# Kernel optimization log

Measured on AMD Instinct MI355X. Metric: run time of the kernel, lower is better.

Reference implementation:

```python
import jax, jax.numpy as jnp
import numpy as np

N_NODES = 100000
IN_DIM = 128
HID = 128
N_REL = 2
N_EDGES = 500000


def setup_inputs() -> dict:
    key = jax.random.key(0)
    ks = jax.random.split(key, 12)
    x = jax.random.normal(ks[0], (N_NODES, IN_DIM), dtype=jnp.float32)
    edge_index = jax.random.randint(ks[1], (2, N_EDGES), 0, N_NODES, dtype=jnp.int64)
    edge_type = jax.random.randint(ks[2], (N_EDGES,), 0, N_REL, dtype=jnp.int64)
    def w(k, shape, fan_in):
        return jax.random.normal(k, shape, dtype=jnp.float32) / np.sqrt(fan_in)
    return {
        "x": x,
        "edge_index": edge_index,
        "edge_type": edge_type,
        "W_rel1": w(ks[3], (N_REL, IN_DIM, HID), IN_DIM),
        "W_root1": w(ks[4], (IN_DIM, HID), IN_DIM),
        "b1": jnp.zeros((HID,), jnp.float32),
        "W_rel2": w(ks[5], (N_REL, HID, HID), HID),
        "W_root2": w(ks[6], (HID, HID), HID),
        "b2": jnp.zeros((HID,), jnp.float32),
        "Wc": w(ks[7], (HID, 2), HID),
        "bc": jnp.zeros((2,), jnp.float32),
    }


def rgcn_conv(x, src, dst, edge_type, W_rel, W_root, b, n_nodes):
    """PyG RGCNConv: out_i = x_i @ W_root + b + sum_r mean_{j in N_r(i)} x_j @ W_r."""
    out = x @ W_root + b
    for r in range(W_rel.shape[0]):  # small fixed relation count
        mask = (edge_type == r).astype(x.dtype)  # [E]
        xr = x @ W_rel[r]                         # [N, dout] transform-then-gather
        msg = xr[src] * mask[:, None]             # [E, dout]
        agg = jax.ops.segment_sum(msg, dst, num_segments=n_nodes)   # [N, dout]
        cnt = jax.ops.segment_sum(mask, dst, num_segments=n_nodes)  # [N]
        out = out + agg / jnp.maximum(cnt, 1.0)[:, None]            # mean aggr
    return out


def reference(x, edge_index, edge_type, W_rel1, W_root1, b1, W_rel2, W_root2, b2, Wc, bc):
    n = x.shape[0]
    src, dst = edge_index[0], edge_index[1]
    h = rgcn_conv(x, src, dst, edge_type, W_rel1, W_root1, b1, n)
    h = jax.nn.relu(h)
    # dropout is identity at inference (training=False)
    h = rgcn_conv(h, src, dst, edge_type, W_rel2, W_root2, b2, n)
    h = jax.nn.relu(h)
    logits = h @ Wc + bc
    return logits
```

## Files before the change

### kernel.cpp

```cpp
#include <hip/hip_runtime.h>
#include <hip/hip_fp16.h>

#define N_NODES 100000
#define PAD_N   100096
#define IN_DIM 128
#define HID 128
#define N_REL 2
#define N_EDGES 500000
#define M_SEG (N_REL * N_NODES)
#define SCAN_BLK 1024
#define SCAN_NB ((M_SEG + SCAN_BLK - 1) / SCAN_BLK)

#define CVT_BLOCKS 12500
#define PACK_BLOCKS 48
#define HIST_BLOCKS 1954

typedef __attribute__((ext_vector_type(8))) _Float16 half8;
typedef __attribute__((ext_vector_type(4))) float float4v;

__device__ __forceinline__ unsigned short f2h(float f) {
    return __half_as_ushort(__float2half(f));
}

__global__ __launch_bounds__(256) void prep_kernel(
    const float* __restrict__ X, unsigned short* __restrict__ Xb,
    const float* __restrict__ Wroot1, const float* __restrict__ Wrel1,
    const float* __restrict__ Wroot2, const float* __restrict__ Wrel2,
    unsigned short* __restrict__ Wp,
    const int* __restrict__ ei, const int* __restrict__ et,
    unsigned* __restrict__ cnt)
{
    int bid = blockIdx.x;
    if (bid < CVT_BLOCKS) {
        int i = bid * 256 + threadIdx.x;
        if (i >= N_NODES * IN_DIM / 4) return;
        float4 v = ((const float4*)X)[i];
        ushort4 o;
        o.x = f2h(v.x); o.y = f2h(v.y); o.z = f2h(v.z); o.w = f2h(v.w);
        ((ushort4*)Xb)[i] = o;
    } else if (bid < CVT_BLOCKS + PACK_BLOCKS) {
        int tid = (bid - CVT_BLOCKS) * 256 + threadIdx.x;
        int layer = tid / 6144;
        int rem   = tid % 6144;
        int ks    = rem / 512;
        int rem2  = rem % 512;
        int nt    = rem2 / 64;
        int lane  = rem2 % 64;
        int seg = ks >> 2;
        int kl  = (ks & 3) * 32 + (lane >> 4) * 8;
        int chan = nt * 16 + (lane & 15);
        const float* Wroot = layer ? Wroot2 : Wroot1;
        const float* Wrel  = layer ? Wrel2  : Wrel1;
        const float* W = (seg == 0) ? Wroot : (Wrel + (size_t)(seg - 1) * 128 * 128);
        unsigned short* dst = Wp + (size_t)tid * 8;
        #pragma unroll
        for (int j = 0; j < 8; ++j)
            dst[j] = f2h(W[(size_t)(kl + j) * 128 + chan]);
    } else {
        int e = (bid - CVT_BLOCKS - PACK_BLOCKS) * 256 + threadIdx.x;
        if (e >= N_EDGES) return;
        int dst = ei[N_EDGES + e];
        int r = et[e];
        atomicAdd(cnt + (size_t)r * N_NODES + dst, 1u);
    }
}

__global__ __launch_bounds__(256) void scan1_kernel(
    const unsigned* __restrict__ cnt,
    unsigned* __restrict__ rs, unsigned* __restrict__ bsums)
{
    __shared__ unsigned sdata[256];
    int t = threadIdx.x;
    int base = blockIdx.x * SCAN_BLK + t * 4;
    unsigned v[4]; unsigned s = 0;
    #pragma unroll
    for (int j = 0; j < 4; ++j) {
        v[j] = (base + j < M_SEG) ? cnt[base + j] : 0u;
        s += v[j];
    }
    sdata[t] = s;
    __syncthreads();
    #pragma unroll
    for (int off = 1; off < 256; off <<= 1) {
        unsigned x = (t >= off) ? sdata[t - off] : 0u;
        __syncthreads();
        if (t >= off) sdata[t] += x;
        __syncthreads();
    }
    unsigned excl = (t > 0) ? sdata[t - 1] : 0u;
    if (t == 255) bsums[blockIdx.x] = sdata[255];
    unsigned run = excl;
    #pragma unroll
    for (int j = 0; j < 4; ++j) {
        if (base + j < M_SEG) rs[base + j] = run;
        run += v[j];
    }
}

__global__ __launch_bounds__(256) void scan2_kernel(unsigned* __restrict__ bsums)
{
    __shared__ unsigned sdata[256];
    int t = threadIdx.x;
    sdata[t] = (t < SCAN_NB) ? bsums[t] : 0u;
    __syncthreads();
    #pragma unroll
    for (int off = 1; off < 256; off <<= 1) {
        unsigned x = (t >= off) ? sdata[t - off] : 0u;
        __syncthreads();
        if (t >= off) sdata[t] += x;
        __syncthreads();
    }
    if (t < SCAN_NB) bsums[t] = (t > 0) ? sdata[t - 1] : 0u;
}

__global__ __launch_bounds__(256) void scan3_kernel(
    unsigned* __restrict__ rs, const unsigned* __restrict__ bsums,
    unsigned* __restrict__ cursor)
{
    int i = blockIdx.x * blockDim.x + threadIdx.x;
    if (i < M_SEG) {
        unsigned v = rs[i] + bsums[i >> 10];
        rs[i] = v;
        cursor[i] = v;
    }
    if (i == 0) rs[M_SEG] = N_EDGES;
}

__global__ __launch_bounds__(256) void fill_kernel(
    const int* __restrict__ ei, const int* __restrict__ et,
    unsigned* __restrict__ cursor, unsigned* __restrict__ csr)
{
    int e = blockIdx.x * blockDim.x + threadIdx.x;
    if (e >= N_EDGES) return;
    int src = ei[e];
    int dst = ei[N_EDGES + e];
    int r = et[e];
    unsigned pos = atomicAdd(cursor + (size_t)r * N_NODES + dst, 1u);
    csr[pos] = (unsigned)src;
}

template <bool FINAL>
__global__ __launch_bounds__(256) void gemm_kernel(
    const unsigned short* __restrict__ Xin,
    const unsigned* __restrict__ rs,
    const unsigned* __restrict__ csr,
    const unsigned short* __restrict__ Wp,
    const float* __restrict__ bias,
    unsigned short* __restrict__ Hout,
    const float* __restrict__ Wc,
    const float* __restrict__ bc,
    float* __restrict__ Out)
{
    const int t    = threadIdx.x;
    const int w    = t >> 6;
    const int lane = t & 63;
    const int l15  = lane & 15;
    const int quad = lane >> 4;
    const int rowbase = blockIdx.x * 64 + w * 16;
    const int koff = quad * 8;

    const uint4* __restrict__ X4 = (const uint4*)Xin;

    const int node = rowbase + l15;
    unsigned p_[2], e_[2]; float inv_[2];
    #pragma unroll
    for (int r = 0; r < 2; ++r) {
        unsigned st = 0, en = 0;
        if (node < N_NODES) {
            unsigned sg = (unsigned)r * N_NODES + (unsigned)node;
            st = rs[sg];
            en = rs[sg + 1];
        }
        p_[r] = st; e_[r] = en;
        unsigned d = en - st;
        inv_[r] = 1.0f / (float)(d ? d : 1u);
    }

    __half2 a2[2][4][4];
    #pragma unroll
    for (int r = 0; r < 2; ++r)
        #pragma unroll
        for (int ksl = 0; ksl < 4; ++ksl)
            #pragma unroll
            for (int j = 0; j < 4; ++j)
                a2[r][ksl][j] = __float2half2_rn(0.f);

    const __half2 one2  = __float2half2_rn(1.f);
    const __half2 zero2 = __float2half2_rn(0.f);

    unsigned id[2][2];
    #pragma unroll
    for (int r = 0; r < 2; ++r)
        #pragma unroll
        for (int s = 0; s < 2; ++s) {
            unsigned q = p_[r] + (unsigned)s;
            id[r][s] = csr[q < e_[r] ? q : 0u];
        }

    while (__any((p_[0] < e_[0]) | (p_[1] < e_[1]))) {
        bool act[2][2];
        #pragma unroll
        for (int r = 0; r < 2; ++r)
            #pragma unroll
            for (int s = 0; s < 2; ++s)
                act[r][s] = (p_[r] + (unsigned)s) < e_[r];

        uint4 v[2][2][4];
        #pragma unroll
        for (int r = 0; r < 2; ++r)
            #pragma unroll
            for (int s = 0; s < 2; ++s) {
                const uint4* row = X4 +
                    ((size_t)(act[r][s] ? id[r][s] : 0u) << 4) + quad;
                v[r][s][0] = row[0];
                v[r][s][1] = row[4];
                v[r][s][2] = row[8];
                v[r][s][3] = row[12];
            }

        unsigned pn[2];
        #pragma unroll
        for (int r = 0; r < 2; ++r) {
            unsigned q = p_[r] + 2u;
            pn[r] = q > e_[r] ? e_[r] : q;
        }
        unsigned idn[2][2];
        #pragma unroll
        for (int r = 0; r < 2; ++r)
            #pragma unroll
            for (int s = 0; s < 2; ++s) {
                unsigned q = pn[r] + (unsigned)s;
                idn[r][s] = csr[q < e_[r] ? q : 0u];
            }

        #pragma unroll
        for (int r = 0; r < 2; ++r)
            #pragma unroll
            for (int s = 0; s < 2; ++s) {
                __half2 m = act[r][s] ? one2 : zero2;
                #pragma unroll
                for (int ksl = 0; ksl < 4; ++ksl)
                    #pragma unroll
                    for (int j = 0; j < 4; ++j)
                        a2[r][ksl][j] = __hfma2(((const __half2*)&v[r][s][ksl])[j],
                                                m, a2[r][ksl][j]);
            }

        #pragma unroll
        for (int r = 0; r < 2; ++r) {
            p_[r] = pn[r];
            #pragma unroll
            for (int s = 0; s < 2; ++s) id[r][s] = idn[r][s];
        }
    }

    half8 ag[2][4];
    #pragma unroll
    for (int r = 0; r < 2; ++r) {
        __half2 s2 = __float2half2_rn(inv_[r]);
        #pragma unroll
        for (int ksl = 0; ksl < 4; ++ksl) {
            half8 h;
            #pragma unroll
            for (int j = 0; j < 4; ++j)
                ((__half2*)&h)[j] = __hmul2(a2[r][ksl][j], s2);
            ag[r][ksl] = h;
        }
    }

    auto ldB = [&](int ks, int nt) -> half8 {
        return *(const half8*)(Wp + ((size_t)(ks * 8 + nt) * 64 + lane) * 8);
    };
    const unsigned short* aBase = Xin + (size_t)(rowbase + l15) * 128 + koff;
    auto ldA = [&](int ks) -> half8 {
        return *(const half8*)(aBase + (ks & 3) * 32);
    };

    float4v acc[8];
    #pragma unroll
    for (int nt = 0; nt < 8; ++nt) {
        float bv = bias[nt * 16 + l15];
        acc[nt] = float4v{bv, bv, bv, bv};
    }

    half8 bb[2][8];
    half8 ax[2];
    #pragma unroll
    for (int nt = 0; nt < 8; ++nt) bb[0][nt] = ldB(0, nt);
    ax[0] = ldA(0);

    #pragma unroll
    for (int ks = 0; ks < 12; ++ks) {
        if (ks + 1 < 12) {
            #pragma unroll
            for (int nt = 0; nt < 8; ++nt)
                bb[(ks + 1) & 1][nt] = ldB(ks + 1, nt);
            if (ks + 1 < 4) ax[(ks + 1) & 1] = ldA(ks + 1);
        }
        half8 A = (ks < 4) ? ax[ks & 1] : ag[(ks >> 2) - 1][ks & 3];
        #pragma unroll
        for (int nt = 0; nt < 8; ++nt)
            acc[nt] = __builtin_amdgcn_mfma_f32_16x16x32_f16(A, bb[ks & 1][nt], acc[nt], 0, 0, 0);
    }

    if (!FINAL) {
        #pragma unroll
        for (int rr = 0; rr < 4; ++rr) {
            int n2 = rowbase + quad * 4 + rr;
            unsigned short* hp = Hout + (size_t)n2 * 128 + l15;
            #pragma unroll
            for (int nt = 0; nt < 8; ++nt)
                hp[nt * 16] = f2h(fmaxf(acc[nt][rr], 0.f));
        }
    } else {
        float wc0[8], wc1[8];
        #pragma unroll
        for (int nt = 0; nt < 8; ++nt) {
            wc0[nt] = Wc[(nt * 16 + l15) * 2 + 0];
            wc1[nt] = Wc[(nt * 16 + l15) * 2 + 1];
        }
        float b0 = bc[0], b1 = bc[1];
        #pragma unroll
        for (int rr = 0; rr < 4; ++rr) {
            float l0 = 0.f, l1 = 0.f;
            #pragma unroll
            for (int nt = 0; nt < 8; ++nt) {
                float h = fmaxf(acc[nt][rr], 0.f);
                l0 += h * wc0[nt];
                l1 += h * wc1[nt];
            }
            #pragma unroll
            for (int off = 8; off > 0; off >>= 1) {
                l0 += __shfl_down(l0, off, 16);
                l1 += __shfl_down(l1, off, 16);
            }
            int n2 = rowbase + quad * 4 + rr;
            if (l15 == 0 && n2 < N_NODES) {
                Out[(size_t)n2 * 2 + 0] = l0 + b0;
                Out[(size_t)n2 * 2 + 1] = l1 + b1;
            }
        }
    }
}

extern "C" void kernel_launch(void* const* d_in, const int* in_sizes, int n_in,
                              void* d_out, int out_size, void* d_ws, size_t ws_size,
                              hipStream_t stream)
{
    const float* x      = (const float*)d_in[0];
    const int*   ei     = (const int*)d_in[1];
    const int*   et     = (const int*)d_in[2];
    const float* Wrel1  = (const float*)d_in[3];
    const float* Wroot1 = (const float*)d_in[4];
    const float* b1     = (const float*)d_in[5];
    const float* Wrel2  = (const float*)d_in[6];
    const float* Wroot2 = (const float*)d_in[7];
    const float* b2     = (const float*)d_in[8];
    const float* Wc     = (const float*)d_in[9];
    const float* bc     = (const float*)d_in[10];
    float* out = (float*)d_out;

    char* ws = (char*)d_ws;
    size_t off = 0;
    auto alloc = [&](size_t bytes) {
        void* p = ws + off;
        off += (bytes + 255) & ~(size_t)255;
        return p;
    };
    unsigned short* xb    = (unsigned short*)alloc((size_t)PAD_N * IN_DIM * 2);
    unsigned short* h1b   = (unsigned short*)alloc((size_t)PAD_N * HID * 2);
    unsigned short* Wp    = (unsigned short*)alloc((size_t)2 * 12 * 8 * 64 * 8 * 2);
    unsigned*       rs    = (unsigned*)alloc((size_t)(M_SEG + 1) * 4);
    unsigned*       cursor= (unsigned*)alloc((size_t)M_SEG * 4);
    unsigned*       bsums = (unsigned*)alloc(256 * 4);
    unsigned*       csr   = (unsigned*)alloc((size_t)N_EDGES * 4);

    const int edge_blocks = (N_EDGES + 255) / 256;
    const int seg_blocks  = (M_SEG + 255) / 256;
    const int gemm_blocks = PAD_N / 64;
    const int prep_blocks = CVT_BLOCKS + PACK_BLOCKS + HIST_BLOCKS;

    hipMemsetAsync(cursor, 0, (size_t)M_SEG * 4, stream);
    prep_kernel<<<prep_blocks, 256, 0, stream>>>(
        x, xb, Wroot1, Wrel1, Wroot2, Wrel2, Wp, ei, et, cursor);
    scan1_kernel<<<SCAN_NB, 256, 0, stream>>>(cursor, rs, bsums);
    scan2_kernel<<<1, 256, 0, stream>>>(bsums);
    scan3_kernel<<<seg_blocks, 256, 0, stream>>>(rs, bsums, cursor);
    fill_kernel<<<edge_blocks, 256, 0, stream>>>(ei, et, cursor, csr);

    gemm_kernel<false><<<gemm_blocks, 256, 0, stream>>>(
        xb, rs, csr, Wp, b1, h1b, nullptr, nullptr, nullptr);

    gemm_kernel<true><<<gemm_blocks, 256, 0, stream>>>(
        h1b, rs, csr, Wp + (size_t)12 * 8 * 64 * 8, b2, nullptr, Wc, bc, out);
}
```

Before: 268.6 us.

## Fuse scan and CSR fill into one kernel with grid-wide atomic barriers

```diff
diff --git a/kernel.cpp b/kernel.cpp
--- a/kernel.cpp
+++ b/kernel.cpp
@@ -9,7 +9,7 @@
 #define N_EDGES 500000
 #define M_SEG (N_REL * N_NODES)
 #define SCAN_BLK 1024
-#define SCAN_NB ((M_SEG + SCAN_BLK - 1) / SCAN_BLK)
+#define CSR_NB ((M_SEG + SCAN_BLK - 1) / SCAN_BLK)
 
 #define CVT_BLOCKS 12500
 #define PACK_BLOCKS 48
@@ -65,17 +65,23 @@
     }
 }
 
-__global__ __launch_bounds__(256) void scan1_kernel(
-    const unsigned* __restrict__ cnt,
-    unsigned* __restrict__ rs, unsigned* __restrict__ bsums)
+__global__ __launch_bounds__(256) void csr_kernel(
+    const int* __restrict__ ei, const int* __restrict__ et,
+    unsigned* __restrict__ cursor,
+    unsigned* __restrict__ rs,
+    unsigned* __restrict__ bsums,
+    unsigned* __restrict__ done,
+    unsigned* __restrict__ csr)
 {
     __shared__ unsigned sdata[256];
-    int t = threadIdx.x;
-    int base = blockIdx.x * SCAN_BLK + t * 4;
+    __shared__ unsigned sb[256];
+    const int b = blockIdx.x, t = threadIdx.x;
+    const int base = b * SCAN_BLK + t * 4;
+
     unsigned v[4]; unsigned s = 0;
     #pragma unroll
     for (int j = 0; j < 4; ++j) {
-        v[j] = (base + j < M_SEG) ? cnt[base + j] : 0u;
+        v[j] = (base + j < M_SEG) ? cursor[base + j] : 0u;
         s += v[j];
     }
     sdata[t] = s;
@@ -87,56 +93,50 @@
         if (t >= off) sdata[t] += x;
         __syncthreads();
     }
+    if (t == 255) {
+        bsums[b] = sdata[255];
+        __threadfence();
+        atomicAdd(done, 1u);
+    }
+    if (t == 0) { while (atomicAdd(done, 0u) < (unsigned)CSR_NB) {} }
+    __syncthreads();
+    __threadfence();
+
+    sb[t] = (t < CSR_NB) ? bsums[t] : 0u;
+    __syncthreads();
+    #pragma unroll
+    for (int off = 1; off < 256; off <<= 1) {
+        unsigned x = (t >= off) ? sb[t - off] : 0u;
+        __syncthreads();
+        if (t >= off) sb[t] += x;
+        __syncthreads();
+    }
+    unsigned goff = (b > 0) ? sb[b - 1] : 0u;
     unsigned excl = (t > 0) ? sdata[t - 1] : 0u;
-    if (t == 255) bsums[blockIdx.x] = sdata[255];
-    unsigned run = excl;
+    unsigned run = goff + excl;
     #pragma unroll
     for (int j = 0; j < 4; ++j) {
-        if (base + j < M_SEG) rs[base + j] = run;
+        if (base + j < M_SEG) { rs[base + j] = run; cursor[base + j] = run; }
         run += v[j];
     }
-}
-
-__global__ __launch_bounds__(256) void scan2_kernel(unsigned* __restrict__ bsums)
-{
-    __shared__ unsigned sdata[256];
-    int t = threadIdx.x;
-    sdata[t] = (t < SCAN_NB) ? bsums[t] : 0u;
-    __syncthreads();
-    #pragma unroll
-    for (int off = 1; off < 256; off <<= 1) {
-        unsigned x = (t >= off) ? sdata[t - off] : 0u;
-        __syncthreads();
-        if (t >= off) sdata[t] += x;
-        __syncthreads();
-    }
-    if (t < SCAN_NB) bsums[t] = (t > 0) ? sdata[t - 1] : 0u;
-}
-
-__global__ __launch_bounds__(256) void scan3_kernel(
-    unsigned* __restrict__ rs, const unsigned* __restrict__ bsums,
-    unsigned* __restrict__ cursor)
-{
-    int i = blockIdx.x * blockDim.x + threadIdx.x;
-    if (i < M_SEG) {
-        unsigned v = rs[i] + bsums[i >> 10];
-        rs[i] = v;
-        cursor[i] = v;
-    }
-    if (i == 0) rs[M_SEG] = N_EDGES;
-}
-
-__global__ __launch_bounds__(256) void fill_kernel(
-    const int* __restrict__ ei, const int* __restrict__ et,
-    unsigned* __restrict__ cursor, unsigned* __restrict__ csr)
-{
-    int e = blockIdx.x * blockDim.x + threadIdx.x;
-    if (e >= N_EDGES) return;
-    int src = ei[e];
-    int dst = ei[N_EDGES + e];
-    int r = et[e];
-    unsigned pos = atomicAdd(cursor + (size_t)r * N_NODES + dst, 1u);
-    csr[pos] = (unsigned)src;
+    if (b == 0 && t == 0) rs[M_SEG] = N_EDGES;
+
+    __threadfence();
+    __syncthreads();
+    if (t == 0) {
+        atomicAdd(done, 1u);
+        while (atomicAdd(done, 0u) < 2u * (unsigned)CSR_NB) {}
+    }
+    __syncthreads();
+    __threadfence();
+
+    for (int e = b * 256 + t; e < N_EDGES; e += CSR_NB * 256) {
+        int src = ei[e];
+        int dst = ei[N_EDGES + e];
+        int r = et[e];
+        unsigned pos = atomicAdd(cursor + (size_t)r * N_NODES + dst, 1u);
+        csr[pos] = (unsigned)src;
+    }
 }
 
 template <bool FINAL>
@@ -372,21 +372,17 @@
     unsigned short* Wp    = (unsigned short*)alloc((size_t)2 * 12 * 8 * 64 * 8 * 2);
     unsigned*       rs    = (unsigned*)alloc((size_t)(M_SEG + 1) * 4);
     unsigned*       cursor= (unsigned*)alloc((size_t)M_SEG * 4);
+    unsigned*       done  = (unsigned*)alloc(256);
     unsigned*       bsums = (unsigned*)alloc(256 * 4);
     unsigned*       csr   = (unsigned*)alloc((size_t)N_EDGES * 4);
 
-    const int edge_blocks = (N_EDGES + 255) / 256;
-    const int seg_blocks  = (M_SEG + 255) / 256;
     const int gemm_blocks = PAD_N / 64;
     const int prep_blocks = CVT_BLOCKS + PACK_BLOCKS + HIST_BLOCKS;
 
-    hipMemsetAsync(cursor, 0, (size_t)M_SEG * 4, stream);
+    hipMemsetAsync(cursor, 0, (size_t)M_SEG * 4 + 256, stream);
     prep_kernel<<<prep_blocks, 256, 0, stream>>>(
         x, xb, Wroot1, Wrel1, Wroot2, Wrel2, Wp, ei, et, cursor);
-    scan1_kernel<<<SCAN_NB, 256, 0, stream>>>(cursor, rs, bsums);
-    scan2_kernel<<<1, 256, 0, stream>>>(bsums);
-    scan3_kernel<<<seg_blocks, 256, 0, stream>>>(rs, bsums, cursor);
-    fill_kernel<<<edge_blocks, 256, 0, stream>>>(ei, et, cursor, csr);
+    csr_kernel<<<CSR_NB, 256, 0, stream>>>(ei, et, cursor, rs, bsums, done, csr);
 
     gemm_kernel<false><<<gemm_blocks, 256, 0, stream>>>(
         xb, rs, csr, Wp, b1, h1b, nullptr, nullptr, nullptr);
```

Result: slower. 332.5 us (+23.8%).
